# Optimization experiments

Measured on AMD Instinct MI355X. Metric: run time of the kernel, lower is better.

The kernel has to match this reference:

```python
import jax, jax.numpy as jnp
import numpy as np

NUM_HEADS = 12

def setup_inputs() -> dict:
    key = jax.random.key(0)
    ks = jax.random.split(key, 6)
    B, N, C = 8, 1024, 768
    H = W = 32
    rel_sp_dim = 2 * H - 1  # 63
    head_dim = C // NUM_HEADS  # 64
    s = 0.02
    return {
        "x": jax.random.normal(ks[0], (B, N, C), dtype=jnp.float32),
        "qkv_w": jax.random.normal(ks[1], (3 * C, C), dtype=jnp.float32) * s,
        "rel_pos_h": jax.random.normal(ks[2], (rel_sp_dim, head_dim), dtype=jnp.float32) * s,
        "rel_pos_w": jax.random.normal(ks[3], (rel_sp_dim, head_dim), dtype=jnp.float32) * s,
        "proj_w": jax.random.normal(ks[4], (C, C), dtype=jnp.float32) * s,
        "proj_b": jax.random.normal(ks[5], (C,), dtype=jnp.float32) * s,
        "H": H,
        "W": W,
    }

def reference(x, qkv_w, rel_pos_h, rel_pos_w, proj_w, proj_b, H, W):
    B, N, C = x.shape
    nh = NUM_HEADS
    hd = C // nh
    scale = hd ** -0.5

    # QKV projection (no bias)
    qkv = (x @ qkv_w.T).reshape(B, N, 3, nh, hd)
    qkv = jnp.transpose(qkv, (2, 0, 3, 1, 4))  # [3, B, nh, N, hd]
    q, k, v = qkv[0] * scale, qkv[1], qkv[2]

    attn = jnp.einsum('bhqd,bhkd->bhqk', q, k)  # [B, nh, N, N]

    # relative position bias (q_shape == k_shape, so ratios are 1)
    dist_h = jnp.arange(H)[:, None] - jnp.arange(H)[None, :] + (H - 1)
    dist_w = jnp.arange(W)[:, None] - jnp.arange(W)[None, :] + (W - 1)
    Rh = rel_pos_h[dist_h]  # [H, H, hd]
    Rw = rel_pos_w[dist_w]  # [W, W, hd]

    r_q = q.reshape(B, nh, H, W, hd)
    rel_h = jnp.einsum('byhwc,hkc->byhwk', r_q, Rh)  # [B, nh, H, W, H]
    rel_w = jnp.einsum('byhwc,wkc->byhwk', r_q, Rw)  # [B, nh, H, W, W]

    attn = attn.reshape(B, nh, H, W, H, W)
    attn = attn + rel_h[:, :, :, :, :, None] + rel_w[:, :, :, :, None, :]
    attn = attn.reshape(B, nh, N, N)

    attn = jax.nn.softmax(attn, axis=-1)
    out = jnp.einsum('bhqk,bhkd->bhqd', attn, v)  # [B, nh, N, hd]
    out = jnp.transpose(out, (0, 2, 1, 3)).reshape(B, N, C)
    return out @ proj_w.T + proj_b
```

## Files before the change

### kernel.cpp

```cpp
#include <hip/hip_runtime.h>

#define DEVI __device__ __forceinline__

typedef float f32x4 __attribute__((ext_vector_type(4)));
typedef float f32x16 __attribute__((ext_vector_type(16)));
typedef short bf16x8 __attribute__((ext_vector_type(8)));
typedef unsigned int uint2v __attribute__((ext_vector_type(2)));

DEVI unsigned short f2bf(float f) {
  union { float f; unsigned int u; } v; v.f = f;
  unsigned int u = v.u;
  u += 0x7fffu + ((u >> 16) & 1u);
  return (unsigned short)(u >> 16);
}
DEVI float bf2f(unsigned short h) {
  union { unsigned int u; float f; } v; v.u = ((unsigned int)h) << 16;
  return v.f;
}

DEVI void gld_lds16(const void* g, void* l) {
  __builtin_amdgcn_global_load_lds(
      (const __attribute__((address_space(1))) void*)g,
      (__attribute__((address_space(3))) void*)l, 16, 0, 0);
}

DEVI unsigned int cvt_pk_bf16(float lo, float hi) {
  unsigned int r;
  asm("v_cvt_pk_bf16_f32 %0, %1, %2" : "=v"(r) : "v"(lo), "v"(hi));
  return r;
}

DEVI float exp2_raw(float x) {
  float r;
  asm("v_exp_f32 %0, %1" : "=v"(r) : "v"(x));
  return r;
}

#define MFMA16(a, b, c) __builtin_amdgcn_mfma_f32_16x16x32_bf16((a), (b), (c), 0, 0, 0)
#define MFMA32(a, b, c) __builtin_amdgcn_mfma_f32_32x32x16_bf16((a), (b), (c), 0, 0, 0)

#define QSCALE 0.18033688011112042f

__global__ void __launch_bounds__(256) convert3_kernel(
    const float* __restrict__ x, const float* __restrict__ qkv_w,
    const float* __restrict__ proj_w,
    unsigned short* __restrict__ xb, unsigned short* __restrict__ wqkv,
    unsigned short* __restrict__ wproj) {
  const int i = blockIdx.x * 256 + threadIdx.x;
  const float* src; unsigned short* dst; int off;
  if (i < 1572864)      { src = x;      dst = xb;    off = i; }
  else if (i < 2015232) { src = qkv_w;  dst = wqkv;  off = i - 1572864; }
  else                  { src = proj_w; dst = wproj; off = i - 2015232; }
  float4 v = ((const float4*)src)[off];
  ushort4 o;
  o.x = f2bf(v.x); o.y = f2bf(v.y); o.z = f2bf(v.z); o.w = f2bf(v.w);
  ((ushort4*)dst)[off] = o;
}

template <int MODE>
__global__ void __launch_bounds__(256) gemm_nt(
    const unsigned short* __restrict__ A,
    const unsigned short* __restrict__ Bw,
    unsigned short* __restrict__ oq,
    unsigned short* __restrict__ okk,
    unsigned short* __restrict__ ovt,
    float* __restrict__ of,
    const float* __restrict__ bias) {
  constexpr int K = 768;
  constexpr int NT = K / 64;
  const int tid = threadIdx.x;
  const int l = tid & 63, wv = tid >> 6;
  const int wy = wv >> 1, wx = wv & 1;
  const int lg = l >> 4, lr = l & 15;
  const int m0 = blockIdx.x * 128, n0 = blockIdx.y * 128;

  __shared__ __align__(16) unsigned short As[2][128 * 64];
  __shared__ __align__(16) unsigned short Bs[2][128 * 64];

  f32x4 acc[4][4] = {};

  auto stage = [&](int buf, int k0) {
#pragma unroll
    for (int c = 0; c < 4; ++c) {
      const int row = c * 32 + wv * 8 + (l >> 3);
      const int g = l & 7;
      const int off = ((g ^ (row & 7)) * 8);
      gld_lds16(A + (size_t)(m0 + row) * K + k0 + off, &As[buf][(c * 32 + wv * 8) * 64]);
      gld_lds16(Bw + (size_t)(n0 + row) * K + k0 + off, &Bs[buf][(c * 32 + wv * 8) * 64]);
    }
  };

  stage(0, 0);

  int cur = 0;
  for (int t = 0; t < NT; ++t) {
    if (t + 1 < NT) {
      stage(cur ^ 1, (t + 1) * 64);
      asm volatile("s_waitcnt vmcnt(8)" ::: "memory");
    } else {
      asm volatile("s_waitcnt vmcnt(0)" ::: "memory");
    }
    __builtin_amdgcn_s_barrier();
    __builtin_amdgcn_sched_barrier(0);

#pragma unroll
    for (int kk = 0; kk < 2; ++kk) {
      bf16x8 af[4], bfr[4];
#pragma unroll
      for (int i = 0; i < 4; ++i) {
        const int row = wy * 64 + i * 16 + lr;
        af[i] = *(const bf16x8*)&As[cur][row * 64 + (((kk * 4 + lg) ^ (row & 7)) * 8)];
      }
#pragma unroll
      for (int j = 0; j < 4; ++j) {
        const int row = wx * 64 + j * 16 + lr;
        bfr[j] = *(const bf16x8*)&Bs[cur][row * 64 + (((kk * 4 + lg) ^ (row & 7)) * 8)];
      }
#pragma unroll
      for (int i = 0; i < 4; ++i) {
#pragma unroll
        for (int j = 0; j < 4; ++j)
          acc[i][j] = MFMA16(af[i], bfr[j], acc[i][j]);
      }
    }

    asm volatile("s_waitcnt lgkmcnt(0)" ::: "memory");
    __builtin_amdgcn_sched_barrier(0);
    __builtin_amdgcn_s_barrier();
    cur ^= 1;
  }

  if constexpr (MODE == 0) {
    const int t = n0 / 768;
    if (t < 2) {
      unsigned short* base = (t == 0) ? oq : okk;
      const float sc = (t == 0) ? QSCALE : 1.0f;
#pragma unroll
      for (int i = 0; i < 4; ++i) {
        const int m = m0 + wy * 64 + i * 16 + lg * 4;
#pragma unroll
        for (int j = 0; j < 4; ++j) {
          const int col = n0 + wx * 64 + j * 16 + lr;
          const int rem = col - t * 768;
          const int h = rem >> 6, d = rem & 63;
#pragma unroll
          for (int r = 0; r < 4; ++r) {
            const int mm = m + r;
            const int b = mm >> 10, n = mm & 1023;
            base[(((size_t)(b * 12 + h) << 10) + n) * 64 + d] = f2bf(acc[i][j][r] * sc);
          }
        }
      }
    } else {
#pragma unroll
      for (int i = 0; i < 4; ++i) {
        const int m = m0 + wy * 64 + i * 16 + lg * 4;
        const int b = m >> 10, ntok = m & 1023;
#pragma unroll
        for (int j = 0; j < 4; ++j) {
          const int col = n0 + wx * 64 + j * 16 + lr;
          const int rem = col - 1536;
          const int h = rem >> 6, d = rem & 63;
          ushort4 pk4;
          pk4.x = f2bf(acc[i][j][0]); pk4.y = f2bf(acc[i][j][1]);
          pk4.z = f2bf(acc[i][j][2]); pk4.w = f2bf(acc[i][j][3]);
          *(ushort4*)(ovt + ((size_t)(b * 12 + h) * 64 + d) * 1024 + ntok) = pk4;
        }
      }
    }
  } else {
#pragma unroll
    for (int i = 0; i < 4; ++i) {
      const int m = m0 + wy * 64 + i * 16 + lg * 4;
#pragma unroll
      for (int j = 0; j < 4; ++j) {
        const int col = n0 + wx * 64 + j * 16 + lr;
        const float bv = bias[col];
#pragma unroll
        for (int r = 0; r < 4; ++r)
          of[(size_t)(m + r) * 768 + col] = acc[i][j][r] + bv;
      }
    }
  }
}

__global__ void __launch_bounds__(256) rel_kernel(
    const unsigned short* __restrict__ Q,
    const float* __restrict__ rph,
    const float* __restrict__ rpw,
    unsigned short* __restrict__ relh_t,
    unsigned short* __restrict__ relw_t) {
  const int bh = blockIdx.y;
  const int tid = threadIdx.x;
  const int l = tid & 63, w = tid >> 6;
  const int hi = l >> 5, l31 = l & 31;
  const int yx = blockIdx.x * 4 + w;

  const unsigned short* Qb = Q + (size_t)bh * 65536;

  f32x16 acch = {};
#pragma unroll
  for (int s4 = 0; s4 < 4; ++s4) {
    const float* ar = rph + (yx + 31 - l31) * 64 + s4 * 16 + hi * 8;
    float4 fa = ((const float4*)ar)[0], fb = ((const float4*)ar)[1];
    union { unsigned int u[4]; bf16x8 v; } au;
    au.u[0] = cvt_pk_bf16(fa.x, fa.y); au.u[1] = cvt_pk_bf16(fa.z, fa.w);
    au.u[2] = cvt_pk_bf16(fb.x, fb.y); au.u[3] = cvt_pk_bf16(fb.z, fb.w);
    bf16x8 qv = *(const bf16x8*)(Qb + (size_t)(yx * 32 + l31) * 64 + s4 * 16 + hi * 8);
    acch = MFMA32(au.v, qv, acch);
  }
  {
    unsigned short* ob = relh_t + (size_t)bh * 32768 + yx * 32 + l31;
#pragma unroll
    for (int r = 0; r < 16; ++r) {
      const int kh = (r & 3) + 8 * (r >> 2) + 4 * hi;
      ob[(size_t)kh * 1024] = f2bf(acch[r]);
    }
  }

  f32x16 accw = {};
#pragma unroll
  for (int s4 = 0; s4 < 4; ++s4) {
    const float* ar = rpw + (yx + 31 - l31) * 64 + s4 * 16 + hi * 8;
    float4 fa = ((const float4*)ar)[0], fb = ((const float4*)ar)[1];
    union { unsigned int u[4]; bf16x8 v; } au;
    au.u[0] = cvt_pk_bf16(fa.x, fa.y); au.u[1] = cvt_pk_bf16(fa.z, fa.w);
    au.u[2] = cvt_pk_bf16(fb.x, fb.y); au.u[3] = cvt_pk_bf16(fb.z, fb.w);
    bf16x8 qv = *(const bf16x8*)(Qb + (size_t)(l31 * 32 + yx) * 64 + s4 * 16 + hi * 8);
    accw = MFMA32(au.v, qv, accw);
  }
  {
    unsigned short* ob = relw_t + (size_t)bh * 32768 + l31 * 32 + yx;
#pragma unroll
    for (int r = 0; r < 16; ++r) {
      const int kw = (r & 3) + 8 * (r >> 2) + 4 * hi;
      ob[(size_t)kw * 1024] = f2bf(accw[r]);
    }
  }
}

__global__ void __launch_bounds__(256, 3) attn_kernel(
    const unsigned short* __restrict__ Q,
    const unsigned short* __restrict__ Km,
    const unsigned short* __restrict__ VT,
    const unsigned short* __restrict__ relh_t,
    const unsigned short* __restrict__ relw_t,
    unsigned short* __restrict__ out) {
  const int bid = blockIdx.x;
  const int qt = bid / 96;
  const int bh = bid % 96;
  const int q0 = qt * 128;
  const int tid = threadIdx.x;
  const int l = tid & 63, w = tid >> 6;
  const int hi = l >> 5, l31 = l & 31;

  __shared__ __align__(16) unsigned short Ks[2][64 * 64];
  __shared__ __align__(16) unsigned short VTs[2][64 * 64];
  __shared__ __align__(16) unsigned short rhsL[32 * 128];

  const unsigned short* Kb = Km + (size_t)bh * 65536;
  const unsigned short* Vb = VT + (size_t)bh * 65536;

#pragma unroll
  for (int c = 0; c < 2; ++c) {
    const int row = c * 16 + w * 4 + (l >> 4);
    gld_lds16(relh_t + (size_t)bh * 32768 + (size_t)row * 1024 + q0 + (l & 15) * 8,
              &rhsL[(c * 16 + w * 4) * 128]);
  }

  auto stage = [&](int buf, int t) {
#pragma unroll
    for (int c = 0; c < 2; ++c) {
      const int row = c * 32 + w * 8 + (l >> 3);
      const int g = l & 7;
      const int off = (g ^ (row & 7)) * 8;
      gld_lds16(Kb + (size_t)(t * 64 + row) * 64 + off, &Ks[buf][(c * 32 + w * 8) * 64]);
      gld_lds16(Vb + (size_t)row * 1024 + t * 64 + off, &VTs[buf][(c * 32 + w * 8) * 64]);
    }
  };

  bf16x8 qf[4];
  {
    const unsigned short* qp =
        Q + (size_t)bh * 65536 + (size_t)(q0 + w * 32 + l31) * 64 + hi * 8;
#pragma unroll
    for (int s4 = 0; s4 < 4; ++s4) qf[s4] = *(const bf16x8*)(qp + s4 * 16);
  }

  f32x16 rwacc;
  bf16x8 onesA;
  {
    bf16x8 idA0, idA1, rwB0, rwB1;
    const short onebf = (short)0x3F80;
#pragma unroll
    for (int e = 0; e < 8; ++e) {
      idA0[e] = (l31 == hi * 8 + e) ? onebf : (short)0;
      idA1[e] = (l31 == 16 + hi * 8 + e) ? onebf : (short)0;
      onesA[e] = onebf;
      rwB0[e] = (short)relw_t[(size_t)bh * 32768 + (size_t)(hi * 8 + e) * 1024 +
                              q0 + w * 32 + l31];
      rwB1[e] = (short)relw_t[(size_t)bh * 32768 + (size_t)(16 + hi * 8 + e) * 1024 +
                              q0 + w * 32 + l31];
    }
    f32x16 z = {};
    rwacc = MFMA32(idA0, rwB0, z);
    rwacc = MFMA32(idA1, rwB1, rwacc);
  }

  f32x16 od0 = {}, od1 = {}, sumacc = {};
  int cur = 0;

  stage(0, 0);
  __syncthreads();

  for (int t = 0; t < 16; ++t) {
    if (t < 15) stage(cur ^ 1, t + 1);

    f32x16 s0, s1;
    {
      const int row0 = l31, row1 = 32 + l31;
      bf16x8 kf0 = *(const bf16x8*)&Ks[cur][row0 * 64 + ((hi ^ (row0 & 7)) * 8)];
      bf16x8 kf1 = *(const bf16x8*)&Ks[cur][row1 * 64 + ((hi ^ (row1 & 7)) * 8)];
      s0 = MFMA32(kf0, qf[0], rwacc);
      s1 = MFMA32(kf1, qf[0], rwacc);
    }
#pragma unroll
    for (int s4 = 1; s4 < 4; ++s4) {
      {
        const int row = l31;
        bf16x8 kf = *(const bf16x8*)&Ks[cur][row * 64 + (((s4 * 2 + hi) ^ (row & 7)) * 8)];
        s0 = MFMA32(kf, qf[s4], s0);
      }
      {
        const int row = 32 + l31;
        bf16x8 kf = *(const bf16x8*)&Ks[cur][row * 64 + (((s4 * 2 + hi) ^ (row & 7)) * 8)];
        s1 = MFMA32(kf, qf[s4], s1);
      }
    }

    const float rh0 = bf2f(rhsL[(2 * t) * 128 + w * 32 + l31]);
    const float rh1 = bf2f(rhsL[(2 * t + 1) * 128 + w * 32 + l31]);
#pragma unroll
    for (int r = 0; r < 16; ++r) {
      s0[r] = exp2_raw(s0[r] + rh0);
      s1[r] = exp2_raw(s1[r] + rh1);
    }

    bf16x8 pa[4];
#pragma unroll
    for (int ks = 0; ks < 4; ++ks) {
      unsigned int c0, c1, c2, c3;
      if (ks == 0) {
        c0 = cvt_pk_bf16(s0[0], s0[1]);  c1 = cvt_pk_bf16(s0[2], s0[3]);
        c2 = cvt_pk_bf16(s0[4], s0[5]);  c3 = cvt_pk_bf16(s0[6], s0[7]);
      } else if (ks == 1) {
        c0 = cvt_pk_bf16(s0[8], s0[9]);  c1 = cvt_pk_bf16(s0[10], s0[11]);
        c2 = cvt_pk_bf16(s0[12], s0[13]); c3 = cvt_pk_bf16(s0[14], s0[15]);
      } else if (ks == 2) {
        c0 = cvt_pk_bf16(s1[0], s1[1]);  c1 = cvt_pk_bf16(s1[2], s1[3]);
        c2 = cvt_pk_bf16(s1[4], s1[5]);  c3 = cvt_pk_bf16(s1[6], s1[7]);
      } else {
        c0 = cvt_pk_bf16(s1[8], s1[9]);  c1 = cvt_pk_bf16(s1[10], s1[11]);
        c2 = cvt_pk_bf16(s1[12], s1[13]); c3 = cvt_pk_bf16(s1[14], s1[15]);
      }
      uint2v x = __builtin_amdgcn_permlane32_swap(c0, c2, false, false);
      uint2v z = __builtin_amdgcn_permlane32_swap(c1, c3, false, false);
      union { unsigned int u[4]; bf16x8 v; } uu;
      uu.u[0] = x.x; uu.u[1] = z.x; uu.u[2] = x.y; uu.u[3] = z.y;
      pa[ks] = uu.v;
    }

#pragma unroll
    for (int ks = 0; ks < 4; ++ks) {
      {
        const int row = l31;
        bf16x8 vf = *(const bf16x8*)&VTs[cur][row * 64 + (((ks * 2 + hi) ^ (row & 7)) * 8)];
        od0 = MFMA32(vf, pa[ks], od0);
      }
      {
        const int row = 32 + l31;
        bf16x8 vf = *(const bf16x8*)&VTs[cur][row * 64 + (((ks * 2 + hi) ^ (row & 7)) * 8)];
        od1 = MFMA32(vf, pa[ks], od1);
      }
      sumacc = MFMA32(onesA, pa[ks], sumacc);
    }

    __syncthreads();
    cur ^= 1;
  }

  const float inv = 1.f / sumacc[0];
  const int b = bh / 12, h = bh % 12;
  const int n = q0 + w * 32 + l31;
  unsigned short* ob = out + ((size_t)(b * 1024 + n)) * 768 + h * 64;
#pragma unroll
  for (int r4 = 0; r4 < 4; ++r4) {
    ushort4 p0, p1;
    p0.x = f2bf(od0[r4 * 4 + 0] * inv); p0.y = f2bf(od0[r4 * 4 + 1] * inv);
    p0.z = f2bf(od0[r4 * 4 + 2] * inv); p0.w = f2bf(od0[r4 * 4 + 3] * inv);
    p1.x = f2bf(od1[r4 * 4 + 0] * inv); p1.y = f2bf(od1[r4 * 4 + 1] * inv);
    p1.z = f2bf(od1[r4 * 4 + 2] * inv); p1.w = f2bf(od1[r4 * 4 + 3] * inv);
    *(ushort4*)(ob + 8 * r4 + 4 * hi) = p0;
    *(ushort4*)(ob + 32 + 8 * r4 + 4 * hi) = p1;
  }
}

extern "C" void kernel_launch(void* const* d_in, const int* in_sizes, int n_in,
                              void* d_out, int out_size, void* d_ws, size_t ws_size,
                              hipStream_t stream) {
  const float* x      = (const float*)d_in[0];
  const float* qkv_w  = (const float*)d_in[1];
  const float* rph    = (const float*)d_in[2];
  const float* rpw    = (const float*)d_in[3];
  const float* proj_w = (const float*)d_in[4];
  const float* proj_b = (const float*)d_in[5];
  float* out = (float*)d_out;

  char* ws = (char*)d_ws;
  unsigned short* xb     = (unsigned short*)(ws);
  unsigned short* wqkv   = (unsigned short*)(ws + 12582912);
  unsigned short* wproj  = (unsigned short*)(ws + 16121856);
  unsigned short* qb     = (unsigned short*)(ws + 17301504);
  unsigned short* kb     = (unsigned short*)(ws + 29884416);
  unsigned short* vbT    = (unsigned short*)(ws + 42467328);
  unsigned short* relh_t = (unsigned short*)(ws + 55050240);
  unsigned short* relw_t = (unsigned short*)(ws + 61341696);

  convert3_kernel<<<8448, 256, 0, stream>>>(x, qkv_w, proj_w, xb, wqkv, wproj);

  gemm_nt<0><<<dim3(64, 18), 256, 0, stream>>>(xb, wqkv, qb, kb, vbT, nullptr, nullptr);

  rel_kernel<<<dim3(8, 96), 256, 0, stream>>>(qb, rph, rpw, relh_t, relw_t);

  attn_kernel<<<768, 256, 0, stream>>>(qb, kb, vbT, relh_t, relw_t, xb);

  gemm_nt<1><<<dim3(64, 6), 256, 0, stream>>>(xb, wproj, nullptr, nullptr, nullptr, out, proj_b);
}
```

Baseline: 140.2 us.

## Load GEMM fragments directly from global memory instead of LDS staging

```diff
diff --git a/kernel.cpp b/kernel.cpp
--- a/kernel.cpp
+++ b/kernel.cpp
@@ -67,67 +67,36 @@
     float* __restrict__ of,
     const float* __restrict__ bias) {
   constexpr int K = 768;
-  constexpr int NT = K / 64;
   const int tid = threadIdx.x;
   const int l = tid & 63, wv = tid >> 6;
   const int wy = wv >> 1, wx = wv & 1;
   const int lg = l >> 4, lr = l & 15;
   const int m0 = blockIdx.x * 128, n0 = blockIdx.y * 128;
 
-  __shared__ __align__(16) unsigned short As[2][128 * 64];
-  __shared__ __align__(16) unsigned short Bs[2][128 * 64];
+  const unsigned short* Ab = A + (size_t)(m0 + wy * 64 + lr) * K + lg * 8;
+  const unsigned short* Bb = Bw + (size_t)(n0 + wx * 64 + lr) * K + lg * 8;
 
   f32x4 acc[4][4] = {};
 
-  auto stage = [&](int buf, int k0) {
-#pragma unroll
-    for (int c = 0; c < 4; ++c) {
-      const int row = c * 32 + wv * 8 + (l >> 3);
-      const int g = l & 7;
-      const int off = ((g ^ (row & 7)) * 8);
-      gld_lds16(A + (size_t)(m0 + row) * K + k0 + off, &As[buf][(c * 32 + wv * 8) * 64]);
-      gld_lds16(Bw + (size_t)(n0 + row) * K + k0 + off, &Bs[buf][(c * 32 + wv * 8) * 64]);
-    }
-  };
-
-  stage(0, 0);
-
-  int cur = 0;
-  for (int t = 0; t < NT; ++t) {
-    if (t + 1 < NT) {
-      stage(cur ^ 1, (t + 1) * 64);
-      asm volatile("s_waitcnt vmcnt(8)" ::: "memory");
-    } else {
-      asm volatile("s_waitcnt vmcnt(0)" ::: "memory");
-    }
-    __builtin_amdgcn_s_barrier();
-    __builtin_amdgcn_sched_barrier(0);
-
+  for (int k0 = 0; k0 < K; k0 += 64) {
+    bf16x8 af[8], bfr[8];
 #pragma unroll
     for (int kk = 0; kk < 2; ++kk) {
-      bf16x8 af[4], bfr[4];
 #pragma unroll
       for (int i = 0; i < 4; ++i) {
-        const int row = wy * 64 + i * 16 + lr;
-        af[i] = *(const bf16x8*)&As[cur][row * 64 + (((kk * 4 + lg) ^ (row & 7)) * 8)];
-      }
-#pragma unroll
-      for (int j = 0; j < 4; ++j) {
-        const int row = wx * 64 + j * 16 + lr;
-        bfr[j] = *(const bf16x8*)&Bs[cur][row * 64 + (((kk * 4 + lg) ^ (row & 7)) * 8)];
-      }
+        af[kk * 4 + i] = *(const bf16x8*)(Ab + (size_t)i * 16 * K + k0 + kk * 32);
+        bfr[kk * 4 + i] = *(const bf16x8*)(Bb + (size_t)i * 16 * K + k0 + kk * 32);
+      }
+    }
+#pragma unroll
+    for (int kk = 0; kk < 2; ++kk) {
 #pragma unroll
       for (int i = 0; i < 4; ++i) {
 #pragma unroll
         for (int j = 0; j < 4; ++j)
-          acc[i][j] = MFMA16(af[i], bfr[j], acc[i][j]);
-      }
-    }
-
-    asm volatile("s_waitcnt lgkmcnt(0)" ::: "memory");
-    __builtin_amdgcn_sched_barrier(0);
-    __builtin_amdgcn_s_barrier();
-    cur ^= 1;
+          acc[i][j] = MFMA16(af[kk * 4 + i], bfr[kk * 4 + j], acc[i][j]);
+      }
+    }
   }
 
   if constexpr (MODE == 0) {
```

Measured after the change: 239.8 us. 71.0% more time.

## Load K/V fragments directly from global memory, dropping LDS staging and barriers

Applied to the files above, without the earlier changes.

```diff
diff --git a/kernel.cpp b/kernel.cpp
--- a/kernel.cpp
+++ b/kernel.cpp
@@ -239,7 +239,7 @@
   }
 }
 
-__global__ void __launch_bounds__(256, 3) attn_kernel(
+__global__ void __launch_bounds__(256, 2) attn_kernel(
     const unsigned short* __restrict__ Q,
     const unsigned short* __restrict__ Km,
     const unsigned short* __restrict__ VT,
@@ -254,30 +254,9 @@
   const int l = tid & 63, w = tid >> 6;
   const int hi = l >> 5, l31 = l & 31;
 
-  __shared__ __align__(16) unsigned short Ks[2][64 * 64];
-  __shared__ __align__(16) unsigned short VTs[2][64 * 64];
-  __shared__ __align__(16) unsigned short rhsL[32 * 128];
-
-  const unsigned short* Kb = Km + (size_t)bh * 65536;
-  const unsigned short* Vb = VT + (size_t)bh * 65536;
-
-#pragma unroll
-  for (int c = 0; c < 2; ++c) {
-    const int row = c * 16 + w * 4 + (l >> 4);
-    gld_lds16(relh_t + (size_t)bh * 32768 + (size_t)row * 1024 + q0 + (l & 15) * 8,
-              &rhsL[(c * 16 + w * 4) * 128]);
-  }
-
-  auto stage = [&](int buf, int t) {
-#pragma unroll
-    for (int c = 0; c < 2; ++c) {
-      const int row = c * 32 + w * 8 + (l >> 3);
-      const int g = l & 7;
-      const int off = (g ^ (row & 7)) * 8;
-      gld_lds16(Kb + (size_t)(t * 64 + row) * 64 + off, &Ks[buf][(c * 32 + w * 8) * 64]);
-      gld_lds16(Vb + (size_t)row * 1024 + t * 64 + off, &VTs[buf][(c * 32 + w * 8) * 64]);
-    }
-  };
+  const unsigned short* Kb = Km + (size_t)bh * 65536 + (size_t)l31 * 64 + hi * 8;
+  const unsigned short* Vb = VT + (size_t)bh * 65536 + (size_t)l31 * 1024 + hi * 8;
+  const unsigned short* rhb = relh_t + (size_t)bh * 32768 + q0 + w * 32 + l31;
 
   bf16x8 qf[4];
   {
@@ -308,38 +287,33 @@
   }
 
   f32x16 od0 = {}, od1 = {}, sumacc = {};
-  int cur = 0;
-
-  stage(0, 0);
-  __syncthreads();
 
   for (int t = 0; t < 16; ++t) {
-    if (t < 15) stage(cur ^ 1, t + 1);
-
-    f32x16 s0, s1;
-    {
-      const int row0 = l31, row1 = 32 + l31;
-      bf16x8 kf0 = *(const bf16x8*)&Ks[cur][row0 * 64 + ((hi ^ (row0 & 7)) * 8)];
-      bf16x8 kf1 = *(const bf16x8*)&Ks[cur][row1 * 64 + ((hi ^ (row1 & 7)) * 8)];
-      s0 = MFMA32(kf0, qf[0], rwacc);
-      s1 = MFMA32(kf1, qf[0], rwacc);
-    }
+    const int kv0 = t << 6;
+
+    bf16x8 kf0[4], kf1[4];
+#pragma unroll
+    for (int s4 = 0; s4 < 4; ++s4) {
+      kf0[s4] = *(const bf16x8*)(Kb + (size_t)kv0 * 64 + s4 * 16);
+      kf1[s4] = *(const bf16x8*)(Kb + (size_t)kv0 * 64 + 2048 + s4 * 16);
+    }
+    bf16x8 vf0[4], vf1[4];
+#pragma unroll
+    for (int ks = 0; ks < 4; ++ks) {
+      vf0[ks] = *(const bf16x8*)(Vb + kv0 + ks * 16);
+      vf1[ks] = *(const bf16x8*)(Vb + 32768 + kv0 + ks * 16);
+    }
+    const float rh0 = bf2f(rhb[(size_t)(2 * t) * 1024]);
+    const float rh1 = bf2f(rhb[(size_t)(2 * t + 1) * 1024]);
+
+    f32x16 s0 = MFMA32(kf0[0], qf[0], rwacc);
+    f32x16 s1 = MFMA32(kf1[0], qf[0], rwacc);
 #pragma unroll
     for (int s4 = 1; s4 < 4; ++s4) {
-      {
-        const int row = l31;
-        bf16x8 kf = *(const bf16x8*)&Ks[cur][row * 64 + (((s4 * 2 + hi) ^ (row & 7)) * 8)];
-        s0 = MFMA32(kf, qf[s4], s0);
-      }
-      {
-        const int row = 32 + l31;
-        bf16x8 kf = *(const bf16x8*)&Ks[cur][row * 64 + (((s4 * 2 + hi) ^ (row & 7)) * 8)];
-        s1 = MFMA32(kf, qf[s4], s1);
-      }
-    }
-
-    const float rh0 = bf2f(rhsL[(2 * t) * 128 + w * 32 + l31]);
-    const float rh1 = bf2f(rhsL[(2 * t + 1) * 128 + w * 32 + l31]);
+      s0 = MFMA32(kf0[s4], qf[s4], s0);
+      s1 = MFMA32(kf1[s4], qf[s4], s1);
+    }
+
 #pragma unroll
     for (int r = 0; r < 16; ++r) {
       s0[r] = exp2_raw(s0[r] + rh0);
@@ -372,21 +346,10 @@
 
 #pragma unroll
     for (int ks = 0; ks < 4; ++ks) {
-      {
-        const int row = l31;
-        bf16x8 vf = *(const bf16x8*)&VTs[cur][row * 64 + (((ks * 2 + hi) ^ (row & 7)) * 8)];
-        od0 = MFMA32(vf, pa[ks], od0);
-      }
-      {
-        const int row = 32 + l31;
-        bf16x8 vf = *(const bf16x8*)&VTs[cur][row * 64 + (((ks * 2 + hi) ^ (row & 7)) * 8)];
-        od1 = MFMA32(vf, pa[ks], od1);
-      }
+      od0 = MFMA32(vf0[ks], pa[ks], od0);
+      od1 = MFMA32(vf1[ks], pa[ks], od1);
       sumacc = MFMA32(onesA, pa[ks], sumacc);
     }
-
-    __syncthreads();
-    cur ^= 1;
   }
 
   const float inv = 1.f / sumacc[0];
```

After: 191.3 us. +36.4%, slower.
